# Optimization experiments

Measured on AMD Instinct MI355X. Metric: run time of the kernel, lower is better.

## Reference

```python
import jax, jax.numpy as jnp
import numpy as np

EMBED_DIM = 768
NUM_HEADS = 12


def setup_inputs() -> dict:
    key = jax.random.key(0)
    ks = jax.random.split(key, 9)
    B, N, C = 16, 1024, EMBED_DIM
    std = 1.0 / np.sqrt(C)
    x = jax.random.normal(ks[0], (B, N, C), dtype=jnp.float32)
    def w(k):
        return jax.random.normal(k, (C, C), dtype=jnp.float32) * std
    def b(k):
        return jax.random.normal(k, (C,), dtype=jnp.float32) * 0.01
    return {
        "x": x,
        "Wq": w(ks[1]), "bq": b(ks[2]),
        "Wk": w(ks[3]), "bk": b(ks[4]),
        "Wv": w(ks[5]), "bv": b(ks[6]),
        "Wo": w(ks[7]), "bo": b(ks[8]),
    }


def reference(x, Wq, bq, Wk, bk, Wv, bv, Wo, bo):
    B, N, C = x.shape
    H = NUM_HEADS
    Dh = C // H
    scale = 1.0 / np.sqrt(Dh)

    q = x @ Wq + bq  # (B, N, C)
    k = x @ Wk + bk
    v = x @ Wv + bv

    # Faithful to the original: (B, N, H, Dh) -> reshape(B*H, N, Dh)
    # WITHOUT transposing, exactly as torch_mla_core does (row-major reshape).
    q2 = q.reshape(B * H, N, Dh)
    k2 = k.reshape(B * H, N, Dh)
    v2 = v.reshape(B * H, N, Dh)

    scores = jnp.einsum('gld,gmd->glm', q2, k2) * scale  # (B*H, N, N)
    attn = jax.nn.softmax(scores, axis=-1)
    ctx2 = jnp.einsum('glm,gmd->gld', attn, v2)  # (B*H, N, Dh)

    ctx = ctx2.reshape(B, H, N, Dh).transpose(0, 2, 1, 3).reshape(B, N, C)
    out = ctx @ Wo + bo
    return out
```

## Files before the change

### kernel.cpp

```cpp
#include <hip/hip_runtime.h>
#include <hip/hip_bf16.h>
#include <cstdint>
#include <cstddef>

typedef unsigned short u16;
typedef __attribute__((ext_vector_type(8))) short s8v;
typedef __attribute__((ext_vector_type(4))) float f4v;
typedef __attribute__((ext_vector_type(8))) u16 u16x8;

#define AS1 __attribute__((address_space(1)))
#define AS3 __attribute__((address_space(3)))

#define BATCH 16
#define SEQ   1024
#define EMBED 768
#define HEADS 12
#define DH    64
#define MTOT  (BATCH*SEQ)

__device__ __forceinline__ u16 f2bf(float f) {
    union { float f; uint32_t u; } v; v.f = f;
    uint32_t r = v.u + 0x7fffu + ((v.u >> 16) & 1u);
    return (u16)(r >> 16);
}

__device__ __forceinline__ void gll16(const u16* g, u16* l) {
    __builtin_amdgcn_global_load_lds((AS1 void*)g, (AS3 void*)l, 16, 0, 0);
}

#define XBLOCKS 12288
__global__ void k_pack(const float* __restrict__ x, u16* __restrict__ xb, int nx,
                       const float* __restrict__ Wq, const float* __restrict__ Wk,
                       const float* __restrict__ Wv, const float* __restrict__ Wo,
                       const float* __restrict__ bq, const float* __restrict__ bk,
                       const float* __restrict__ bv,
                       u16* __restrict__ wqkvT, u16* __restrict__ woT,
                       float* __restrict__ bqkv)
{
    if (blockIdx.x < XBLOCKS) {
        int i = (blockIdx.x * 256 + threadIdx.x) * 4;
        if (i + 3 < nx) {
            float4 f = *(const float4*)(x + i);
            ushort4 o;
            o.x = f2bf(f.x); o.y = f2bf(f.y); o.z = f2bf(f.z); o.w = f2bf(f.w);
            *(ushort4*)(xb + i) = o;
        }
        return;
    }
    const int NQKV = 2304 * 768;
    const int NO = 768 * 768;
    int t = (blockIdx.x - XBLOCKS) * 256 + threadIdx.x;
    if (t < NQKV) {
        int n = t % 2304, k = t / 2304;
        const float* src; int nn; float sc;
        if (n < 768)       { src = Wq; nn = n;        sc = 0.125f; }
        else if (n < 1536) { src = Wk; nn = n - 768;  sc = 1.0f;   }
        else               { src = Wv; nn = n - 1536; sc = 1.0f;   }
        wqkvT[(size_t)n * 768 + k] = f2bf(src[(size_t)k * 768 + nn] * sc);
    } else if (t < NQKV + NO) {
        int t2 = t - NQKV;
        int n = t2 % 768, k = t2 / 768;
        woT[(size_t)n * 768 + k] = f2bf(Wo[(size_t)k * 768 + n]);
    } else if (t < NQKV + NO + 2304) {
        int t3 = t - NQKV - NO;
        bqkv[t3] = (t3 < 768) ? bq[t3] * 0.125f
                 : ((t3 < 1536) ? bk[t3 - 768] : bv[t3 - 1536]);
    }
}

template<int MODE>
__global__ __launch_bounds__(256) void k_gemm(
    const u16* __restrict__ A, const u16* __restrict__ BT,
    const float* __restrict__ bias,
    u16* __restrict__ oq, u16* __restrict__ okk, u16* __restrict__ ov,
    float* __restrict__ of)
{
    __shared__ __attribute__((aligned(16))) u16 As[128 * 32];
    __shared__ __attribute__((aligned(16))) u16 Bs[128 * 32];
    const int tid = threadIdx.x;
    const int m0 = blockIdx.x * 128;
    const int n0 = blockIdx.y * 128;
    const int wv = tid >> 6;
    const int ln = tid & 63;
    const int l15 = ln & 15, quad = ln >> 4;
    const int wm = (wv >> 1) * 64, wn = (wv & 1) * 64;
    const int r = tid >> 2, c8 = (tid & 3) * 8;

    const u16* gA0 = A + (size_t)(m0 + r) * 768 + c8;
    const u16* gA1 = gA0 + 64 * 768;
    const u16* gB0 = BT + (size_t)(n0 + r) * 768 + c8;
    const u16* gB1 = gB0 + 64 * 768;
    u16* lA0 = As + wv * 512;
    u16* lA1 = As + 2048 + wv * 512;
    u16* lB0 = Bs + wv * 512;
    u16* lB1 = Bs + 2048 + wv * 512;

    f4v acc[4][4] = {};

    for (int kt = 0; kt < 24; ++kt) {
        const int ko = kt * 32;
        gll16(gA0 + ko, lA0);
        gll16(gA1 + ko, lA1);
        gll16(gB0 + ko, lB0);
        gll16(gB1 + ko, lB1);
        __syncthreads();
        s8v aF[4], bF[4];
#pragma unroll
        for (int i = 0; i < 4; ++i)
            aF[i] = *(const s8v*)(As + (wm + i * 16 + l15) * 32 + quad * 8);
#pragma unroll
        for (int j = 0; j < 4; ++j)
            bF[j] = *(const s8v*)(Bs + (wn + j * 16 + l15) * 32 + quad * 8);
#pragma unroll
        for (int i = 0; i < 4; ++i)
#pragma unroll
            for (int j = 0; j < 4; ++j)
                acc[i][j] = __builtin_amdgcn_mfma_f32_16x16x32_bf16(aF[i], bF[j], acc[i][j], 0, 0, 0);
        __syncthreads();
    }

#pragma unroll
    for (int j = 0; j < 4; ++j) {
        int n = n0 + wn + j * 16 + l15;
        float bs = bias[n];
        if (MODE == 0) {
            u16* dst; int nn;
            if (n < 768)       { dst = oq;  nn = n; }
            else if (n < 1536) { dst = okk; nn = n - 768; }
            else               { dst = ov;  nn = n - 1536; }
#pragma unroll
            for (int i = 0; i < 4; ++i) {
                int mrow = m0 + wm + i * 16 + quad * 4;
#pragma unroll
                for (int rg = 0; rg < 4; ++rg)
                    dst[(size_t)(mrow + rg) * 768 + nn] = f2bf(acc[i][j][rg] + bs);
            }
        } else {
#pragma unroll
            for (int i = 0; i < 4; ++i) {
                int mrow = m0 + wm + i * 16 + quad * 4;
#pragma unroll
                for (int rg = 0; rg < 4; ++rg)
                    of[(size_t)(mrow + rg) * 768 + n] = acc[i][j][rg] + bs;
            }
        }
    }
}

__global__ void k_transpose_v(const u16* __restrict__ v, u16* __restrict__ vt) {
    __shared__ __attribute__((aligned(16))) u16 ts[64 * 80];
    int g = blockIdx.x >> 4;
    int l0 = (blockIdx.x & 15) << 6;
    const u16* vg = v + (size_t)g * 65536;
    u16* vtg = vt + (size_t)g * 65536;
    int tid = threadIdx.x;
#pragma unroll
    for (int c = tid; c < 512; c += 256) {
        int l = c >> 3, d0 = (c & 7) * 8;
        *(uint4*)(ts + l * 80 + d0) = *(const uint4*)(vg + (size_t)(l0 + l) * 64 + d0);
    }
    __syncthreads();
#pragma unroll
    for (int c = tid; c < 512; c += 256) {
        int d = c >> 3, lc = (c & 7) * 8;
        u16x8 tv;
#pragma unroll
        for (int i = 0; i < 8; ++i) tv[i] = ts[(lc + i) * 80 + d];
        *(u16x8*)(vtg + (size_t)d * 1024 + l0 + lc) = tv;
    }
}

#define KS2(r_, c_) ( ((r_) << 6) + (((((c_) >> 3) ^ ((r_) & 7)) & 7) << 3) + ((c_) & 7) )
#define PS_OFF(q_, c_) ( ((q_) << 7) + ((((((c_) >> 3) ^ ((((q_) >> 2) & 3) << 1)) & 15) << 3) | ((c_) & 7)) )

__global__ __launch_bounds__(256) void k_attn(
    const u16* __restrict__ qb, const u16* __restrict__ kb,
    const u16* __restrict__ vt, u16* __restrict__ ctx)
{
    __shared__ __attribute__((aligned(16))) u16 Ks[128 * 64];
    __shared__ __attribute__((aligned(16))) u16 Vts[64 * 136];
    __shared__ __attribute__((aligned(16))) u16 U[64 * 128];

    const int g = blockIdx.x >> 4;
    const int q0 = (blockIdx.x & 15) << 6;
    const int tid = threadIdx.x, wv = tid >> 6;
    const int ln = tid & 63, l15 = ln & 15, quad = ln >> 4;
    const u16* qg = qb + (size_t)g * 65536;
    const u16* kg = kb + (size_t)g * 65536;
    const u16* vtg = vt + (size_t)g * 65536;

#pragma unroll
    for (int c = tid; c < 512; c += 256) {
        int rr = c >> 3, d0 = (c & 7) * 8;
        *(uint4*)(U + rr * 72 + d0) = *(const uint4*)(qg + (size_t)(q0 + rr) * 64 + d0);
    }
    __syncthreads();
    s8v aQ0 = *(const s8v*)(U + (wv * 16 + l15) * 72 + quad * 8);
    s8v aQ1 = *(const s8v*)(U + (wv * 16 + l15) * 72 + 32 + quad * 8);

    f4v o[4] = {};
    float rsum[4] = {0.f, 0.f, 0.f, 0.f};

    for (int jt = 0; jt < 8; ++jt) {
        const int n0 = jt * 128;
        __syncthreads();

#pragma unroll
        for (int i = 0; i < 4; ++i) {
            int t = tid + i * 256;
            int rr = t >> 3, cb = (t & 7) << 3;
            *(uint4*)(Ks + KS2(rr, cb)) = *(const uint4*)(kg + (size_t)(n0 + rr) * 64 + cb);
        }
#pragma unroll
        for (int c = tid; c < 1024; c += 256) {
            int d = c >> 4, c0 = (c & 15) * 8;
            *(uint4*)(Vts + d * 136 + c0) = *(const uint4*)(vtg + (size_t)d * 1024 + n0 + c0);
        }
        __syncthreads();

        f4v s[8];
#pragma unroll
        for (int ns = 0; ns < 8; ++ns) {
            int rK = ns * 16 + l15;
            s8v b0 = *(const s8v*)(Ks + KS2(rK, quad * 8));
            s8v b1 = *(const s8v*)(Ks + KS2(rK, quad * 8 + 32));
            f4v t = {};
            t = __builtin_amdgcn_mfma_f32_16x16x32_bf16(aQ0, b0, t, 0, 0, 0);
            t = __builtin_amdgcn_mfma_f32_16x16x32_bf16(aQ1, b1, t, 0, 0, 0);
            s[ns] = t;
        }

#pragma unroll
        for (int ns = 0; ns < 8; ++ns)
#pragma unroll
            for (int rg = 0; rg < 4; ++rg) {
                float p = __expf(s[ns][rg]);
                s[ns][rg] = p;
                rsum[rg] += p;
            }

#pragma unroll
        for (int ns = 0; ns < 8; ++ns)
#pragma unroll
            for (int rg = 0; rg < 4; ++rg) {
                int q = wv * 16 + quad * 4 + rg;
                U[PS_OFF(q, ns * 16 + l15)] = f2bf(s[ns][rg]);
            }

#pragma unroll
        for (int ks = 0; ks < 4; ++ks) {
            int m = wv * 16 + l15;
            int blk = ks * 4 + quad;
            int sw = ((l15 >> 2) & 3) << 1;
            s8v aP = *(const s8v*)(U + (m << 7) + (((blk ^ sw) & 15) << 3));
#pragma unroll
            for (int ds = 0; ds < 4; ++ds) {
                s8v bV = *(const s8v*)(Vts + (ds * 16 + l15) * 136 + ks * 32 + quad * 8);
                o[ds] = __builtin_amdgcn_mfma_f32_16x16x32_bf16(aP, bV, o[ds], 0, 0, 0);
            }
        }
    }

#pragma unroll
    for (int rg = 0; rg < 4; ++rg) {
        float v = rsum[rg];
        v += __shfl_xor(v, 1, 64);
        v += __shfl_xor(v, 2, 64);
        v += __shfl_xor(v, 4, 64);
        v += __shfl_xor(v, 8, 64);
        rsum[rg] = v;
    }

    const int b = g / 12, h = g % 12;
    u16* cbase = ctx + (size_t)b * 786432 + h * 64;
#pragma unroll
    for (int rg = 0; rg < 4; ++rg) {
        float inv = 1.0f / rsum[rg];
        int row = q0 + wv * 16 + quad * 4 + rg;
#pragma unroll
        for (int ds = 0; ds < 4; ++ds)
            cbase[(size_t)row * 768 + ds * 16 + l15] = f2bf(o[ds][rg] * inv);
    }
}

extern "C" void kernel_launch(void* const* d_in, const int* in_sizes, int n_in,
                              void* d_out, int out_size, void* d_ws, size_t ws_size,
                              hipStream_t stream) {
    const float* x  = (const float*)d_in[0];
    const float* Wq = (const float*)d_in[1];
    const float* bq = (const float*)d_in[2];
    const float* Wk = (const float*)d_in[3];
    const float* bk = (const float*)d_in[4];
    const float* Wv = (const float*)d_in[5];
    const float* bv = (const float*)d_in[6];
    const float* Wo = (const float*)d_in[7];
    const float* bo = (const float*)d_in[8];
    float* out = (float*)d_out;

    const size_t NTOK = (size_t)MTOT * EMBED;
    char* w = (char*)d_ws;
    u16* xb    = (u16*)w;              w += NTOK * 2;
    u16* qb    = (u16*)w;              w += NTOK * 2;
    u16* kb    = (u16*)w;              w += NTOK * 2;
    u16* vb    = (u16*)w;              w += NTOK * 2;
    u16* vtb   = (u16*)w;              w += NTOK * 2;
    u16* wqkvT = (u16*)w;              w += (size_t)2304 * 768 * 2;
    u16* woT   = (u16*)w;              w += (size_t)768 * 768 * 2;
    float* bqkv = (float*)w;           w += 2304 * 4;
    u16* ctx = xb;

    k_pack<<<XBLOCKS + 9225, 256, 0, stream>>>(x, xb, (int)NTOK,
        Wq, Wk, Wv, Wo, bq, bk, bv, wqkvT, woT, bqkv);

    dim3 g1(128, 18);
    k_gemm<0><<<g1, 256, 0, stream>>>(xb, wqkvT, bqkv, qb, kb, vb, nullptr);

    k_transpose_v<<<3072, 256, 0, stream>>>(vb, vtb);
    k_attn<<<3072, 256, 0, stream>>>(qb, kb, vtb, ctx);

    dim3 g2(128, 6);
    k_gemm<1><<<g2, 256, 0, stream>>>(ctx, woT, bo, nullptr, nullptr, nullptr, out);
}
```

Before: 377.3 us.

## Register-prefetch K/V tiles and keep P in registers via permlane swaps

The attention kernel now prefetches the next K and V^T tiles into registers while the current tile is being computed. It computes S transposed so the exp'd probabilities can be packed to bf16 and rearranged across lanes with permlane swaps, which removes the LDS round-trip for P and the U buffer. Q is loaded straight from global memory, and setprio hints plus a min-blocks launch bound are added. In exchange the kernel holds more registers, and the hand-written lane permutation and row-sum shuffle mapping must be exactly right for the output to stay correct.

```diff
diff --git a/kernel.cpp b/kernel.cpp
--- a/kernel.cpp
+++ b/kernel.cpp
@@ -171,15 +171,13 @@
 }
 
 #define KS2(r_, c_) ( ((r_) << 6) + (((((c_) >> 3) ^ ((r_) & 7)) & 7) << 3) + ((c_) & 7) )
-#define PS_OFF(q_, c_) ( ((q_) << 7) + ((((((c_) >> 3) ^ ((((q_) >> 2) & 3) << 1)) & 15) << 3) | ((c_) & 7)) )
-
-__global__ __launch_bounds__(256) void k_attn(
+
+__global__ __launch_bounds__(256, 4) void k_attn(
     const u16* __restrict__ qb, const u16* __restrict__ kb,
     const u16* __restrict__ vt, u16* __restrict__ ctx)
 {
     __shared__ __attribute__((aligned(16))) u16 Ks[128 * 64];
     __shared__ __attribute__((aligned(16))) u16 Vts[64 * 136];
-    __shared__ __attribute__((aligned(16))) u16 U[64 * 128];
 
     const int g = blockIdx.x >> 4;
     const int q0 = (blockIdx.x & 15) << 6;
@@ -189,46 +187,55 @@
     const u16* kg = kb + (size_t)g * 65536;
     const u16* vtg = vt + (size_t)g * 65536;
 
-#pragma unroll
-    for (int c = tid; c < 512; c += 256) {
-        int rr = c >> 3, d0 = (c & 7) * 8;
-        *(uint4*)(U + rr * 72 + d0) = *(const uint4*)(qg + (size_t)(q0 + rr) * 64 + d0);
-    }
-    __syncthreads();
-    s8v aQ0 = *(const s8v*)(U + (wv * 16 + l15) * 72 + quad * 8);
-    s8v aQ1 = *(const s8v*)(U + (wv * 16 + l15) * 72 + 32 + quad * 8);
+    const u16* qrow = qg + (size_t)(q0 + wv * 16 + l15) * 64 + quad * 8;
+    s8v aQ0 = *(const s8v*)qrow;
+    s8v aQ1 = *(const s8v*)(qrow + 32);
+
+    const int krr = tid >> 3, kcb = (tid & 7) * 8;
+    const int vd = tid >> 4, vc0 = (tid & 15) * 8;
+    const u16* kgp = kg + (size_t)krr * 64 + kcb;
+    const u16* vgp = vtg + (size_t)vd * 1024 + vc0;
+
+    uint4 kreg[4], vreg[4];
+#pragma unroll
+    for (int i = 0; i < 4; ++i) kreg[i] = *(const uint4*)(kgp + i * 2048);
+#pragma unroll
+    for (int i = 0; i < 4; ++i) vreg[i] = *(const uint4*)(vgp + i * 16384);
 
     f4v o[4] = {};
-    float rsum[4] = {0.f, 0.f, 0.f, 0.f};
+    float rsum = 0.f;
 
     for (int jt = 0; jt < 8; ++jt) {
-        const int n0 = jt * 128;
         __syncthreads();
-
-#pragma unroll
-        for (int i = 0; i < 4; ++i) {
-            int t = tid + i * 256;
-            int rr = t >> 3, cb = (t & 7) << 3;
-            *(uint4*)(Ks + KS2(rr, cb)) = *(const uint4*)(kg + (size_t)(n0 + rr) * 64 + cb);
-        }
-#pragma unroll
-        for (int c = tid; c < 1024; c += 256) {
-            int d = c >> 4, c0 = (c & 15) * 8;
-            *(uint4*)(Vts + d * 136 + c0) = *(const uint4*)(vtg + (size_t)d * 1024 + n0 + c0);
+#pragma unroll
+        for (int i = 0; i < 4; ++i)
+            *(uint4*)(Ks + KS2(krr + i * 32, kcb)) = kreg[i];
+#pragma unroll
+        for (int i = 0; i < 4; ++i)
+            *(uint4*)(Vts + (vd + i * 16) * 136 + vc0) = vreg[i];
+        if (jt < 7) {
+            const size_t koff = (size_t)(jt + 1) * 8192;
+            const int voff = (jt + 1) * 128;
+#pragma unroll
+            for (int i = 0; i < 4; ++i) kreg[i] = *(const uint4*)(kgp + koff + i * 2048);
+#pragma unroll
+            for (int i = 0; i < 4; ++i) vreg[i] = *(const uint4*)(vgp + voff + i * 16384);
         }
         __syncthreads();
 
         f4v s[8];
+        __builtin_amdgcn_s_setprio(1);
 #pragma unroll
         for (int ns = 0; ns < 8; ++ns) {
             int rK = ns * 16 + l15;
             s8v b0 = *(const s8v*)(Ks + KS2(rK, quad * 8));
             s8v b1 = *(const s8v*)(Ks + KS2(rK, quad * 8 + 32));
             f4v t = {};
-            t = __builtin_amdgcn_mfma_f32_16x16x32_bf16(aQ0, b0, t, 0, 0, 0);
-            t = __builtin_amdgcn_mfma_f32_16x16x32_bf16(aQ1, b1, t, 0, 0, 0);
+            t = __builtin_amdgcn_mfma_f32_16x16x32_bf16(b0, aQ0, t, 0, 0, 0);
+            t = __builtin_amdgcn_mfma_f32_16x16x32_bf16(b1, aQ1, t, 0, 0, 0);
             s[ns] = t;
         }
+        __builtin_amdgcn_s_setprio(0);
 
 #pragma unroll
         for (int ns = 0; ns < 8; ++ns)
@@ -236,46 +243,42 @@
             for (int rg = 0; rg < 4; ++rg) {
                 float p = __expf(s[ns][rg]);
                 s[ns][rg] = p;
-                rsum[rg] += p;
+                rsum += p;
             }
 
-#pragma unroll
-        for (int ns = 0; ns < 8; ++ns)
-#pragma unroll
-            for (int rg = 0; rg < 4; ++rg) {
-                int q = wv * 16 + quad * 4 + rg;
-                U[PS_OFF(q, ns * 16 + l15)] = f2bf(s[ns][rg]);
-            }
-
+        __builtin_amdgcn_s_setprio(1);
 #pragma unroll
         for (int ks = 0; ks < 4; ++ks) {
-            int m = wv * 16 + l15;
-            int blk = ks * 4 + quad;
-            int sw = ((l15 >> 2) & 3) << 1;
-            s8v aP = *(const s8v*)(U + (m << 7) + (((blk ^ sw) & 15) << 3));
+            uint32_t a0, a1, c0, c1;
+            asm("v_cvt_pk_bf16_f32 %0, %1, %2" : "=v"(a0) : "v"(s[2*ks][0]),   "v"(s[2*ks][1]));
+            asm("v_cvt_pk_bf16_f32 %0, %1, %2" : "=v"(a1) : "v"(s[2*ks][2]),   "v"(s[2*ks][3]));
+            asm("v_cvt_pk_bf16_f32 %0, %1, %2" : "=v"(c0) : "v"(s[2*ks+1][0]), "v"(s[2*ks+1][1]));
+            asm("v_cvt_pk_bf16_f32 %0, %1, %2" : "=v"(c1) : "v"(s[2*ks+1][2]), "v"(s[2*ks+1][3]));
+            asm("v_permlane32_swap_b32 %0, %1" : "+v"(a0), "+v"(c0));
+            asm("v_permlane16_swap_b32 %0, %1" : "+v"(a0), "+v"(c0));
+            asm("v_permlane32_swap_b32 %0, %1" : "+v"(a1), "+v"(c1));
+            asm("v_permlane16_swap_b32 %0, %1" : "+v"(a1), "+v"(c1));
+            union { uint4 u; s8v v; } pw;
+            pw.u.x = a0; pw.u.y = a1; pw.u.z = c0; pw.u.w = c1;
+            s8v aP = pw.v;
 #pragma unroll
             for (int ds = 0; ds < 4; ++ds) {
                 s8v bV = *(const s8v*)(Vts + (ds * 16 + l15) * 136 + ks * 32 + quad * 8);
                 o[ds] = __builtin_amdgcn_mfma_f32_16x16x32_bf16(aP, bV, o[ds], 0, 0, 0);
             }
         }
-    }
-
-#pragma unroll
-    for (int rg = 0; rg < 4; ++rg) {
-        float v = rsum[rg];
-        v += __shfl_xor(v, 1, 64);
-        v += __shfl_xor(v, 2, 64);
-        v += __shfl_xor(v, 4, 64);
-        v += __shfl_xor(v, 8, 64);
-        rsum[rg] = v;
-    }
+        __builtin_amdgcn_s_setprio(0);
+    }
+
+    rsum += __shfl_xor(rsum, 16, 64);
+    rsum += __shfl_xor(rsum, 32, 64);
 
     const int b = g / 12, h = g % 12;
     u16* cbase = ctx + (size_t)b * 786432 + h * 64;
 #pragma unroll
     for (int rg = 0; rg < 4; ++rg) {
-        float inv = 1.0f / rsum[rg];
+        float rs = __shfl(rsum, 20 * quad + rg, 64);
+        float inv = 1.0f / rs;
         int row = q0 + wv * 16 + quad * 4 + rg;
 #pragma unroll
         for (int ds = 0; ds < 4; ++ds)
```

Result: slower. 474.0 us (+25.6%).
